# Kernel tuning notes

Measured on AMD Instinct MI355X. Metric: run time of the kernel, lower is better.

The kernel has to match this reference:

```python
import jax, jax.numpy as jnp
import numpy as np

B, N = 4, 20                        # batch, qubits
L = int(np.ceil(np.log2(N)))        # 5 layers, one 4x4 generator each


def setup_inputs():
    key = jax.random.key(0)
    k1, k2, k3, k4 = jax.random.split(key, 4)
    psi_re = jax.random.normal(k1, (B, 2 ** N), dtype=jnp.float32)
    psi_im = jax.random.normal(k2, (B, 2 ** N), dtype=jnp.float32)
    nrm = jnp.sqrt(jnp.sum(psi_re ** 2 + psi_im ** 2, axis=1, keepdims=True))
    psi_re, psi_im = psi_re / nrm, psi_im / nrm   # normalized quantum state
    H_re = jax.random.normal(k3, (L, 4, 4), dtype=jnp.float32)
    H_im = jax.random.normal(k4, (L, 4, 4), dtype=jnp.float32)
    return {"psi_re": psi_re, "psi_im": psi_im, "H_re": H_re, "H_im": H_im}


def _make_unitary(A):
    # torch.matrix_exp(A - A^H): expm of an anti-Hermitian generator via eigh
    G = A - A.conj().T
    w, V = jnp.linalg.eigh(-1j * G)            # G = i * Hermitian
    return (V * jnp.exp(1j * w)) @ V.conj().T  # expm(G), unitary


def _apply_gate(T, U4, axes):
    # contract 4x4 gate (reshaped [2,2,2,2]) onto two qubit axes of tensor T
    T = jnp.tensordot(U4, T, axes=((2, 3), axes))
    return jnp.moveaxis(T, (0, 1), axes)


def _gate_pairs(nq):
    pairs = [(2 * i, 2 * i + 1) for i in range(nq // 2)]
    if nq > 2:
        pairs += [(2 * i + 1, (2 * i + 2) % nq) for i in range(nq // 2)]
    return pairs


def _forward(psi_re, psi_im, H_re, H_im):
    psi = (psi_re + 1j * psi_im).astype(jnp.complex64).reshape((B,) + (2,) * N)
    H = (H_re + 1j * H_im).astype(jnp.complex64)
    state, is_dm, nq = psi, False, N
    for layer in range(L):
        U = _make_unitary(H[layer]).reshape(2, 2, 2, 2)
        Uc = U.conj()
        # _2local_conv: brick pattern of the same 2-qubit gate
        for (a, b) in _gate_pairs(nq):
            state = _apply_gate(state, U, (1 + a, 1 + b))
            if is_dm:  # density matrix: also apply U* on bra axes
                state = _apply_gate(state, Uc, (1 + nq + a, 1 + nq + b))
        # _2local_pool: measuring qubits 0..nq//2-1 with index shifting removes
        # the even-indexed qubits -> partial trace over them
        if nq >= 2:
            traced = [2 * i for i in range(nq // 2)]
            kept = [q for q in range(nq) if q not in traced]
            t, k = len(traced), len(kept)
            if is_dm:
                perm = (0,) + tuple(1 + q for q in kept) + tuple(1 + q for q in traced) \
                     + tuple(1 + nq + q for q in kept) + tuple(1 + nq + q for q in traced)
                r = jnp.transpose(state, perm).reshape(B, 2 ** k, 2 ** t, 2 ** k, 2 ** t)
                state = jnp.einsum('bitjt->bij', r).reshape((B,) + (2,) * k + (2,) * k)
            else:
                perm = (0,) + tuple(1 + q for q in traced) + tuple(1 + q for q in kept)
                p = jnp.transpose(state, perm).reshape(B, 2 ** t, 2 ** k)
                state = jnp.einsum('bti,btj->bij', p, p.conj()).reshape((B,) + (2,) * k + (2,) * k)
                is_dm = True
            nq = k
    # final state.measure(0): reduced 1-qubit density matrix, take P(outcome 0)
    r = state.reshape(B, 2, 2 ** (nq - 1), 2, 2 ** (nq - 1))
    rho0 = jnp.einsum('birjr->bij', r)
    return rho0[:, 0, 0].real


def reference(psi_re, psi_im, H_re, H_im):
    return _forward(psi_re, psi_im, H_re, H_im)
```

## Files before the change

kernel.cpp:

```cpp
#include <hip/hip_runtime.h>
#include <math.h>


typedef float cpx __attribute__((ext_vector_type(2)));

__device__ __forceinline__ cpx mkc(float x, float y) { cpx r; r.x = x; r.y = y; return r; }

__device__ __forceinline__ cpx cmul(cpx a, cpx b) {
  cpx r = a.xx * b;
  return __builtin_elementwise_fma(mkc(-a.y, a.y), b.yx, r);
}
__device__ __forceinline__ cpx cmadd(cpx acc, cpx a, cpx b) {
  acc = __builtin_elementwise_fma(a.xx, b, acc);
  return __builtin_elementwise_fma(mkc(-a.y, a.y), b.yx, acc);
}
__device__ __forceinline__ cpx cmaddc(cpx acc, cpx a, cpx b) {
  acc = __builtin_elementwise_fma(a.xx, mkc(b.x, -b.y), acc);
  return __builtin_elementwise_fma(a.yy, b.yx, acc);
}

__device__ __forceinline__ int pad(int e) { return e + (e >> 4); }
__device__ __forceinline__ int ins(int x, int p) {
  return ((x >> p) << (p + 1)) | (x & ((1 << p) - 1));
}

#define S_STR 36
#define T_STR 1153

__device__ __forceinline__ void gate4(cpx& v0, cpx& v1, cpx& v2, cpx& v3,
                                      const cpx (&U)[16]) {
  cpx n0 = cmul(U[0], v0);  n0 = cmadd(n0, U[1], v1);  n0 = cmadd(n0, U[2], v2);  n0 = cmadd(n0, U[3], v3);
  cpx n1 = cmul(U[4], v0);  n1 = cmadd(n1, U[5], v1);  n1 = cmadd(n1, U[6], v2);  n1 = cmadd(n1, U[7], v3);
  cpx n2 = cmul(U[8], v0);  n2 = cmadd(n2, U[9], v1);  n2 = cmadd(n2, U[10], v2); n2 = cmadd(n2, U[11], v3);
  cpx n3 = cmul(U[12], v0); n3 = cmadd(n3, U[13], v1); n3 = cmadd(n3, U[14], v2); n3 = cmadd(n3, U[15], v3);
  v0 = n0; v1 = n1; v2 = n2; v3 = n3;
}

template <int NG>
__device__ __forceinline__ void gate16n(cpx (&v)[16], const cpx (&U)[16]) {
#pragma unroll
  for (int g = 0; g < 4; g++)
    gate4(v[g * 4 + 0], v[g * 4 + 1], v[g * 4 + 2], v[g * 4 + 3], U);
#pragma unroll
  for (int lo = 0; lo < 4; lo++)
    gate4(v[lo], v[lo + 4], v[lo + 8], v[lo + 12], U);
  if (NG == 3) {
#pragma unroll
    for (int b3 = 0; b3 < 2; b3++)
#pragma unroll
      for (int b0 = 0; b0 < 2; b0++) {
        int j = b3 * 8 + b0;
        gate4(v[j], v[j + 2], v[j + 4], v[j + 6], U);
      }
  }
}

__device__ __forceinline__ void apply_gate_2it(cpx* t, const cpx (&U)[16],
                                               int pa, int pb, int tid) {
  int p0 = pa < pb ? pa : pb;
  int p1 = pa < pb ? pb : pa;
  int m0 = (1 << p0) - 1, m1 = (1 << p1) - 1;
  int ia = 1 << pa, ib = 1 << pb;
#pragma unroll
  for (int g = tid; g < 2048; g += 1024) {
    int idx = ((g & ~m0) << 1) | (g & m0);
    idx = ((idx & ~m1) << 1) | (idx & m1);
    int e0 = pad(idx), e1 = pad(idx | ib), e2 = pad(idx | ia), e3 = pad(idx | ia | ib);
    cpx v0 = t[e0], v1 = t[e1], v2 = t[e2], v3 = t[e3];
    gate4(v0, v1, v2, v3, U);
    t[e0] = v0; t[e1] = v1; t[e2] = v2; t[e3] = v3;
  }
}

__device__ __forceinline__ void phase3_eo(cpx* t, const cpx (&U)[16],
                                          int q0, int q1, int q2,
                                          int o0, int o1, int o2, int tid) {
  int idx = ins(ins(ins(tid, q0), q1), q2);
  cpx v[8];
#pragma unroll
  for (int j = 0; j < 8; j++) {
    int off = ((j & 1) ? o0 : 0) + ((j & 2) ? o1 : 0) + ((j & 4) ? o2 : 0);
    v[j] = t[pad(idx + off)];
  }
  gate4(v[0], v[2], v[4], v[6], U);
  gate4(v[1], v[3], v[5], v[7], U);
  gate4(v[0], v[1], v[2], v[3], U);
  gate4(v[4], v[5], v[6], v[7], U);
#pragma unroll
  for (int j = 0; j < 8; j++) {
    int off = ((j & 1) ? o0 : 0) + ((j & 2) ? o1 : 0) + ((j & 4) ? o2 : 0);
    t[pad(idx + off)] = v[j];
  }
}

template <int NG>
__device__ __forceinline__ void phase4_pool(cpx* w, const cpx (&U)[16],
                                            int a_lo, int a_hi, int c_lo, int c_hi,
                                            int o0, int o1, int o2, int o3, int tid) {
  int uu = tid & 7, ss = (tid >> 3) & 7, t_lo = tid >> 6;
  int u = ins(ins(uu, a_lo), a_hi);
  int s = ins(ins(ss, c_lo), c_hi);
  int base = t_lo * T_STR + s * S_STR + u;
  cpx v[16];
#pragma unroll
  for (int j = 0; j < 16; j++) {
    int off = ((j & 1) ? o0 : 0) + ((j & 2) ? o1 : 0) + ((j & 4) ? o2 : 0) + ((j & 8) ? o3 : 0);
    v[j] = w[base + off];
  }
  gate16n<NG>(v, U);
#pragma unroll
  for (int j = 0; j < 16; j++) {
    int off = ((j & 1) ? o0 : 0) + ((j & 2) ? o1 : 0) + ((j & 4) ? o2 : 0) + ((j & 8) ? o3 : 0);
    w[base + off] = v[j];
  }
}

__device__ __forceinline__ void pool_p3(cpx* w, const cpx (&U)[16], int tid) {
#pragma unroll
  for (int it = 0; it < 2; it++) {
    int h = tid + it * 512;
    int t_lo = h & 7, ss = (h >> 3) & 15, uu = (h >> 7) & 7;
    int base = t_lo * T_STR + (ss << 1) * S_STR + (uu << 2);
    cpx v[8];
    v[0] = w[base];          v[1] = w[base + 1];
    v[4] = w[base + 2];      v[5] = w[base + 3];
    v[2] = w[base + S_STR];      v[3] = w[base + S_STR + 1];
    v[6] = w[base + S_STR + 2];  v[7] = w[base + S_STR + 3];
    gate4(v[0], v[1], v[2], v[3], U);
    gate4(v[4], v[5], v[6], v[7], U);
    gate4(v[0], v[2], v[4], v[6], U);
    gate4(v[1], v[3], v[5], v[7], U);
    w[base] = v[0];          w[base + 1] = v[1];
    w[base + 2] = v[4];      w[base + 3] = v[5];
    w[base + S_STR] = v[2];      w[base + S_STR + 1] = v[3];
    w[base + S_STR + 2] = v[6];  w[base + S_STR + 3] = v[7];
  }
}

__device__ __forceinline__ cpx expm16(const float* __restrict__ Hre,
                                      const float* __restrict__ Him,
                                      int l, int l16) {
  int r = l16 >> 2, c = l16 & 3;
  double tr = (double)Hre[l * 16 + r * 4 + c] - (double)Hre[l * 16 + c * 4 + r];
  double ti = (double)Him[l * 16 + r * 4 + c] + (double)Him[l * 16 + c * 4 + r];
  double a = sqrt(tr * tr + ti * ti);
  a += __shfl_xor(a, 1, 16);
  a += __shfl_xor(a, 2, 16);
  double nrm = fmax(a, __shfl_xor(a, 4, 16));
  nrm = fmax(nrm, __shfl_xor(nrm, 8, 16));
  int s = 0;
  while (nrm > 0.25 && s < 60) { nrm *= 0.5; s++; }
  double sc = ldexp(1.0, -s);
  tr *= sc; ti *= sc;
  double id = (r == c) ? 1.0 : 0.0;
  double er = id, ei = 0.0, pr = id, pi = 0.0;
  for (int k = 1; k <= 16; k++) {
    double qr = 0.0, qi = 0.0;
#pragma unroll
    for (int m = 0; m < 4; m++) {
      double pmr = __shfl(pr, r * 4 + m, 16);
      double pmi = __shfl(pi, r * 4 + m, 16);
      double tmr = __shfl(tr, m * 4 + c, 16);
      double tmi = __shfl(ti, m * 4 + c, 16);
      qr = fma(pmr, tmr, fma(-pmi, tmi, qr));
      qi = fma(pmr, tmi, fma(pmi, tmr, qi));
    }
    double inv = 1.0 / (double)k;
    pr = qr * inv; pi = qi * inv;
    er += pr; ei += pi;
  }
  for (int it = 0; it < s; it++) {
    double qr = 0.0, qi = 0.0;
#pragma unroll
    for (int m = 0; m < 4; m++) {
      double amr = __shfl(er, r * 4 + m, 16);
      double ami = __shfl(ei, r * 4 + m, 16);
      double bmr = __shfl(er, m * 4 + c, 16);
      double bmi = __shfl(ei, m * 4 + c, 16);
      qr = fma(amr, bmr, fma(-ami, bmi, qr));
      qi = fma(amr, bmi, fma(ami, bmr, qi));
    }
    er = qr; ei = qi;
  }
  return mkc((float)er, (float)ei);
}

__global__ __launch_bounds__(128) void compute_U(const float* __restrict__ Hre,
                                                 const float* __restrict__ Him,
                                                 cpx* __restrict__ Umat) {
  int tid = threadIdx.x;
  if (tid < 80) {
    int layer = tid >> 4, l16 = tid & 15;
    Umat[layer * 16 + l16] = expm16(Hre, Him, layer, l16);
  }
}

__global__ __launch_bounds__(1024, 8) void l0_pass1(const float* __restrict__ pre,
                                                    const float* __restrict__ pim,
                                                    const cpx* __restrict__ Umat,
                                                    cpx* __restrict__ state) {
  extern __shared__ cpx tile[];
  int tid = threadIdx.x;
  int bid = blockIdx.x;
  int b = bid >> 7, hi = bid & 127;
  size_t base = ((size_t)b << 20) | ((size_t)hi << 13);
  float4 re[2], im[2];
#pragma unroll
  for (int k = 0; k < 2; k++) {
    int e = (tid + (k << 10)) << 2;
    re[k] = *(const float4*)&pre[base + e];
    im[k] = *(const float4*)&pim[base + e];
  }
#pragma unroll
  for (int k = 0; k < 2; k++) {
    int e = (tid + (k << 10)) << 2;
    int d = pad(e);
    tile[d]     = mkc(re[k].x, im[k].x);
    tile[d + 1] = mkc(re[k].y, im[k].y);
    tile[d + 2] = mkc(re[k].z, im[k].z);
    tile[d + 3] = mkc(re[k].w, im[k].w);
  }
  cpx U[16];
#pragma unroll
  for (int k = 0; k < 16; k++) U[k] = Umat[k];
  __syncthreads();
  apply_gate_2it(tile, U, 1, 0, tid);                 __syncthreads();
  phase3_eo(tile, U, 1, 2, 3, 2, 4, 8, tid);          __syncthreads();
  phase3_eo(tile, U, 3, 4, 5, 8, 16, 32, tid);        __syncthreads();
  phase3_eo(tile, U, 5, 6, 7, 32, 64, 128, tid);      __syncthreads();
  phase3_eo(tile, U, 7, 8, 9, 128, 256, 512, tid);    __syncthreads();
  phase3_eo(tile, U, 9, 10, 11, 512, 1024, 2048, tid);__syncthreads();
  int hifix = ((hi & 1) << 16) | (((hi >> 1) & 1) << 6) | (((hi >> 2) & 1) << 17)
            | (((hi >> 3) & 1) << 5) | (((hi >> 4) & 1) << 18) | (((hi >> 5) & 1) << 7)
            | (((hi >> 6) & 1) << 19);
  size_t dbase = ((size_t)b << 20) | (unsigned)hifix;
  cpx x[8];
#pragma unroll
  for (int k = 0; k < 2; k++) {
    int src = pad((tid + (k << 10)) << 2);
    x[4 * k + 0] = tile[src];     x[4 * k + 1] = tile[src + 1];
    x[4 * k + 2] = tile[src + 2]; x[4 * k + 3] = tile[src + 3];
  }
#pragma unroll
  for (int k = 0; k < 2; k++) {
    int le = tid + (k << 10);
    int d = ((le & 1) << 2) | (((le >> 1) & 1) << 3) | (((le >> 2) & 1) << 8)
          | (((le >> 3) & 1) << 12) | (((le >> 4) & 1) << 10) | (((le >> 5) & 1) << 13)
          | (((le >> 6) & 1) << 9) | (((le >> 7) & 1) << 14) | (((le >> 8) & 1) << 11)
          | (((le >> 9) & 1) << 15) | (((le >> 10) & 1) << 4);
    float4* dst = (float4*)&state[dbase + d];
    dst[0] = make_float4(x[4 * k].x, x[4 * k].y, x[4 * k + 1].x, x[4 * k + 1].y);
    dst[1] = make_float4(x[4 * k + 2].x, x[4 * k + 2].y, x[4 * k + 3].x, x[4 * k + 3].y);
  }
}

__global__ __launch_bounds__(1024, 8) void l0_pass2(const cpx* __restrict__ Umat,
                                                    cpx* __restrict__ state) {
  extern __shared__ cpx tile[];
  int tid = threadIdx.x;
  int bid = blockIdx.x;
  int b = bid >> 7, mid = bid & 127;
  size_t base = ((size_t)b << 20) | ((size_t)mid << 8);
  cpx U[16];
#pragma unroll
  for (int k = 0; k < 16; k++) U[k] = Umat[k];
  {
    float4 v[4];
#pragma unroll
    for (int k = 0; k < 4; k++) {
      int f = tid + (k << 10);
      int run = f >> 7, idx = f & 127;
      v[k] = *(const float4*)&state[base + ((size_t)run << 15) + ((size_t)idx << 1)];
    }
#pragma unroll
    for (int k = 0; k < 4; k++) {
      int f = tid + (k << 10);
      int d = pad((f >> 7) * 256 + (f & 127) * 2);
      tile[d] = mkc(v[k].x, v[k].y);
      tile[d + 1] = mkc(v[k].z, v[k].w);
    }
  }
  __syncthreads();
  phase3_eo(tile, U, 4, 8, 9, 256, 16, 512, tid);     __syncthreads();
  phase3_eo(tile, U, 6, 9, 10, 512, 64, 1024, tid);   __syncthreads();
  phase3_eo(tile, U, 5, 10, 11, 1024, 32, 2048, tid); __syncthreads();
  phase3_eo(tile, U, 7, 11, 12, 2048, 128, 4096, tid);__syncthreads();
  apply_gate_2it(tile, U, 0, 12, tid);                __syncthreads();
  {
    cpx y[8];
#pragma unroll
    for (int k = 0; k < 4; k++) {
      int f = tid + (k << 10);
      int d = pad((f >> 7) * 256 + (f & 127) * 2);
      y[2 * k] = tile[d];
      y[2 * k + 1] = tile[d + 1];
    }
#pragma unroll
    for (int k = 0; k < 4; k++) {
      int f = tid + (k << 10);
      int run = f >> 7, idx = f & 127;
      size_t a = base + ((size_t)run << 15) + ((size_t)idx << 1);
      *(float4*)&state[a] = make_float4(y[2 * k].x, y[2 * k].y, y[2 * k + 1].x, y[2 * k + 1].y);
    }
  }
}

__global__ __launch_bounds__(512, 4) void pool_l1(const cpx* __restrict__ Umat,
                                                  const cpx* __restrict__ state,
                                                  float4* __restrict__ partial) {
  extern __shared__ cpx w[];
  int tid = threadIdx.x;
  int bid = blockIdx.x;
  int b = bid >> 7, thi = bid & 127;
  size_t base = ((size_t)b << 20) | ((size_t)thi << 13);
  cpx U[16];
#pragma unroll
  for (int k = 0; k < 16; k++) U[k] = Umat[16 + k];
  {
    float4 v[8];
#pragma unroll
    for (int k = 0; k < 8; k++) {
      int e = (tid + (k << 9)) << 1;
      v[k] = *(const float4*)&state[base + e];
    }
#pragma unroll
    for (int k = 0; k < 8; k++) {
      int e = (tid + (k << 9)) << 1;
      int u = (((e >> 8) & 1) << 1) | (((e >> 9) & 1) << 2) | (((e >> 4) & 1) << 3) | (((e >> 5) & 1) << 4);
      int s = ((e >> 2) & 1) | (((e >> 10) & 1) << 1) | (((e >> 11) & 1) << 2)
            | (((e >> 6) & 1) << 3) | (((e >> 7) & 1) << 4);
      int t = ((e >> 1) & 1) | (((e >> 3) & 1) << 1) | (((e >> 12) & 1) << 2);
      int c = t * T_STR + s * S_STR + u;
      w[c] = mkc(v[k].x, v[k].y);
      w[c + 1] = mkc(v[k].z, v[k].w);
    }
  }
  __syncthreads();
  phase4_pool<3>(w, U, 3, 4, 3, 4, 8, 8 * S_STR, 16, 16 * S_STR, tid); __syncthreads();
  phase4_pool<3>(w, U, 1, 2, 1, 2, 2, 2 * S_STR, 4, 4 * S_STR, tid);   __syncthreads();
  pool_p3(w, U, tid);                                                  __syncthreads();
  phase4_pool<2>(w, U, 0, 3, 2, 4, 4 * S_STR, 8, 16 * S_STR, 1, tid);  __syncthreads();
  int wv = tid >> 6, lane = tid & 63;
  int u0 = (lane >> 3) << 2, v0 = (lane & 7) << 2;
  cpx acc[4][4];
#pragma unroll
  for (int i = 0; i < 4; i++)
#pragma unroll
    for (int j = 0; j < 4; j++) acc[i][j] = mkc(0.f, 0.f);
  {
    int tb = wv * T_STR;
#pragma unroll 4
    for (int s = 0; s < 32; s++) {
      int row = tb + s * S_STR;
      cpx x[4], y[4];
#pragma unroll
      for (int i = 0; i < 4; i++) { x[i] = w[row + u0 + i]; y[i] = w[row + v0 + i]; }
#pragma unroll
      for (int i = 0; i < 4; i++)
#pragma unroll
        for (int j = 0; j < 4; j++) acc[i][j] = cmaddc(acc[i][j], x[i], y[j]);
    }
  }
  __syncthreads();
#pragma unroll
  for (int i = 0; i < 4; i++)
#pragma unroll
    for (int j = 0; j < 4; j++)
      w[wv * 1024 + (u0 + i) * 32 + (v0 + j)] = acc[i][j];
  __syncthreads();
  {
    cpx s0 = mkc(0.f, 0.f), s1 = mkc(0.f, 0.f);
#pragma unroll
    for (int k = 0; k < 8; k++) {
      s0 += w[k * 1024 + 2 * tid];
      s1 += w[k * 1024 + 2 * tid + 1];
    }
    partial[((size_t)bid << 9) | tid] = make_float4(s0.x, s0.y, s1.x, s1.y);
  }
}

__global__ __launch_bounds__(256) void finish(const cpx* __restrict__ Umat,
                                              const float4* __restrict__ accv,
                                              float* __restrict__ out) {
  __shared__ cpx rho[1024];
  __shared__ cpx r3s[64];
  __shared__ cpx r4s[16];
  int tid = threadIdx.x;
  int b = blockIdx.x;
  float4* rf = (float4*)rho;
  for (int f = tid; f < 512; f += 256) {
    float4 acc = make_float4(0.f, 0.f, 0.f, 0.f);
#pragma unroll 8
    for (int h = 0; h < 128; h++) {
      float4 v = accv[(size_t)(b * 128 + h) * 512 + f];
      acc.x += v.x; acc.y += v.y; acc.z += v.z; acc.w += v.w;
    }
    rf[f] = acc;
  }
  __syncthreads();

  cpx U[16], Uc[16];
#pragma unroll
  for (int k = 0; k < 16; k++) { U[k] = Umat[32 + k]; Uc[k] = mkc(U[k].x, -U[k].y); }
  const int gl2[4][2] = {{4,3},{2,1},{3,2},{1,0}};
#pragma unroll
  for (int gi = 0; gi < 4; gi++) {
    int pa = gl2[gi][0], pb = gl2[gi][1];
    int p0 = pa < pb ? pa : pb, p1 = pa < pb ? pb : pa;
    int m0 = (1 << p0) - 1, m1 = (1 << p1) - 1;
    int ia = 1 << pa, ib = 1 << pb;
    {
      int j = tid >> 3, g = tid & 7;
      int idx = ((g & ~m0) << 1) | (g & m0);
      idx = ((idx & ~m1) << 1) | (idx & m1);
      cpx v0 = rho[idx * 32 + j], v1 = rho[(idx | ib) * 32 + j];
      cpx v2 = rho[(idx | ia) * 32 + j], v3 = rho[(idx | ia | ib) * 32 + j];
      gate4(v0, v1, v2, v3, U);
      rho[idx * 32 + j] = v0; rho[(idx | ib) * 32 + j] = v1;
      rho[(idx | ia) * 32 + j] = v2; rho[(idx | ia | ib) * 32 + j] = v3;
    }
    __syncthreads();
    {
      int i = tid >> 3, g = tid & 7;
      int idx = ((g & ~m0) << 1) | (g & m0);
      idx = ((idx & ~m1) << 1) | (idx & m1);
      cpx v0 = rho[i * 32 + idx], v1 = rho[i * 32 + (idx | ib)];
      cpx v2 = rho[i * 32 + (idx | ia)], v3 = rho[i * 32 + (idx | ia | ib)];
      gate4(v0, v1, v2, v3, Uc);
      rho[i * 32 + idx] = v0; rho[i * 32 + (idx | ib)] = v1;
      rho[i * 32 + (idx | ia)] = v2; rho[i * 32 + (idx | ia | ib)] = v3;
    }
    __syncthreads();
  }
  if (tid < 64) {
    int u = tid >> 3, v = tid & 7;
    cpx acc = mkc(0.f, 0.f);
#pragma unroll
    for (int s = 0; s < 4; s++) {
      int iu = ((s >> 1) << 4) | ((u >> 2) << 3) | ((s & 1) << 2) | (((u >> 1) & 1) << 1) | (u & 1);
      int iv = ((s >> 1) << 4) | ((v >> 2) << 3) | ((s & 1) << 2) | (((v >> 1) & 1) << 1) | (v & 1);
      cpx x = rho[iu * 32 + iv];
      acc.x += x.x; acc.y += x.y;
    }
    r3s[u * 8 + v] = acc;
  }
  __syncthreads();

#pragma unroll
  for (int k = 0; k < 16; k++) { U[k] = Umat[48 + k]; Uc[k] = mkc(U[k].x, -U[k].y); }
  const int gl3[2][2] = {{2,1},{1,0}};
#pragma unroll
  for (int gi = 0; gi < 2; gi++) {
    int pa = gl3[gi][0], pb = gl3[gi][1];
    int p0 = pa < pb ? pa : pb, p1 = pa < pb ? pb : pa;
    int m0 = (1 << p0) - 1, m1 = (1 << p1) - 1;
    int ia = 1 << pa, ib = 1 << pb;
    if (tid < 16) {
      int j = tid >> 1, g = tid & 1;
      int idx = ((g & ~m0) << 1) | (g & m0);
      idx = ((idx & ~m1) << 1) | (idx & m1);
      cpx v0 = r3s[idx * 8 + j], v1 = r3s[(idx | ib) * 8 + j];
      cpx v2 = r3s[(idx | ia) * 8 + j], v3 = r3s[(idx | ia | ib) * 8 + j];
      gate4(v0, v1, v2, v3, U);
      r3s[idx * 8 + j] = v0; r3s[(idx | ib) * 8 + j] = v1;
      r3s[(idx | ia) * 8 + j] = v2; r3s[(idx | ia | ib) * 8 + j] = v3;
    }
    __syncthreads();
    if (tid < 16) {
      int i = tid >> 1, g = tid & 1;
      int idx = ((g & ~m0) << 1) | (g & m0);
      idx = ((idx & ~m1) << 1) | (idx & m1);
      cpx v0 = r3s[i * 8 + idx], v1 = r3s[i * 8 + (idx | ib)];
      cpx v2 = r3s[i * 8 + (idx | ia)], v3 = r3s[i * 8 + (idx | ia | ib)];
      gate4(v0, v1, v2, v3, Uc);
      r3s[i * 8 + idx] = v0; r3s[i * 8 + (idx | ib)] = v1;
      r3s[i * 8 + (idx | ia)] = v2; r3s[i * 8 + (idx | ia | ib)] = v3;
    }
    __syncthreads();
  }
  if (tid < 16) {
    int u = tid >> 2, v = tid & 3;
    cpx acc = mkc(0.f, 0.f);
#pragma unroll
    for (int s = 0; s < 2; s++) {
      cpx x = r3s[((s << 2) | u) * 8 + ((s << 2) | v)];
      acc.x += x.x; acc.y += x.y;
    }
    r4s[u * 4 + v] = acc;
  }
  __syncthreads();

#pragma unroll
  for (int k = 0; k < 16; k++) { U[k] = Umat[64 + k]; Uc[k] = mkc(U[k].x, -U[k].y); }
  if (tid < 4) {
    int j = tid;
    cpx v0 = r4s[0 * 4 + j], v1 = r4s[1 * 4 + j], v2 = r4s[2 * 4 + j], v3 = r4s[3 * 4 + j];
    gate4(v0, v1, v2, v3, U);
    r4s[0 * 4 + j] = v0; r4s[1 * 4 + j] = v1; r4s[2 * 4 + j] = v2; r4s[3 * 4 + j] = v3;
  }
  __syncthreads();
  if (tid < 4) {
    int i = tid;
    cpx v0 = r4s[i * 4 + 0], v1 = r4s[i * 4 + 1], v2 = r4s[i * 4 + 2], v3 = r4s[i * 4 + 3];
    gate4(v0, v1, v2, v3, Uc);
    r4s[i * 4 + 0] = v0; r4s[i * 4 + 1] = v1; r4s[i * 4 + 2] = v2; r4s[i * 4 + 3] = v3;
  }
  __syncthreads();
  if (tid == 0) out[b] = r4s[0].x + r4s[10].x;
}

extern "C" void kernel_launch(void* const* d_in, const int* in_sizes, int n_in,
                              void* d_out, int out_size, void* d_ws, size_t ws_size,
                              hipStream_t stream) {
  const float* psi_re = (const float*)d_in[0];
  const float* psi_im = (const float*)d_in[1];
  const float* H_re = (const float*)d_in[2];
  const float* H_im = (const float*)d_in[3];
  float* out = (float*)d_out;

  char* ws = (char*)d_ws;
  cpx* Umat = (cpx*)ws;
  cpx* state = (cpx*)(ws + 4096);
  float4* partial = (float4*)(ws + 4096 + ((size_t)1 << 25));

  const size_t LDS_L0 = 8704 * sizeof(cpx);
  const size_t LDS_POOL = 8 * T_STR * sizeof(cpx);

  hipLaunchKernelGGL(compute_U, dim3(1), dim3(128), 0, stream, H_re, H_im, Umat);
  hipLaunchKernelGGL(l0_pass1, dim3(512), dim3(1024), LDS_L0, stream,
                     psi_re, psi_im, (const cpx*)Umat, state);
  hipLaunchKernelGGL(l0_pass2, dim3(512), dim3(1024), LDS_L0, stream,
                     (const cpx*)Umat, state);
  hipLaunchKernelGGL(pool_l1, dim3(512), dim3(512), LDS_POOL, stream,
                     (const cpx*)Umat, (const cpx*)state, partial);
  hipLaunchKernelGGL(finish, dim3(4), dim3(256), 0, stream,
                     (const cpx*)Umat, (const float4*)partial, out);
}
```

Measured before the change: 175.9 us.

## Process two tiles per block in layer-0 passes, prefetching the second tile's loads

Both layer-0 kernels now launch 256 blocks, and each block handles two tiles instead of one. The global loads for the second tile are issued into registers before the first tile's gate phases start, so their latency can hide behind LDS compute. This costs extra live registers and lowers the launch-bounds occupancy hint from 8 to 4. With 256 blocks on the device there is also less parallelism to go around.

```diff
diff --git a/kernel.cpp b/kernel.cpp
--- a/kernel.cpp
+++ b/kernel.cpp
@@ -195,41 +195,17 @@
   }
 }
 
-__global__ __launch_bounds__(1024, 8) void l0_pass1(const float* __restrict__ pre,
-                                                    const float* __restrict__ pim,
-                                                    const cpx* __restrict__ Umat,
-                                                    cpx* __restrict__ state) {
-  extern __shared__ cpx tile[];
-  int tid = threadIdx.x;
-  int bid = blockIdx.x;
-  int b = bid >> 7, hi = bid & 127;
-  size_t base = ((size_t)b << 20) | ((size_t)hi << 13);
-  float4 re[2], im[2];
-#pragma unroll
-  for (int k = 0; k < 2; k++) {
-    int e = (tid + (k << 10)) << 2;
-    re[k] = *(const float4*)&pre[base + e];
-    im[k] = *(const float4*)&pim[base + e];
-  }
-#pragma unroll
-  for (int k = 0; k < 2; k++) {
-    int e = (tid + (k << 10)) << 2;
-    int d = pad(e);
-    tile[d]     = mkc(re[k].x, im[k].x);
-    tile[d + 1] = mkc(re[k].y, im[k].y);
-    tile[d + 2] = mkc(re[k].z, im[k].z);
-    tile[d + 3] = mkc(re[k].w, im[k].w);
-  }
-  cpx U[16];
-#pragma unroll
-  for (int k = 0; k < 16; k++) U[k] = Umat[k];
-  __syncthreads();
+__device__ __forceinline__ void p1_phases(cpx* tile, const cpx (&U)[16], int tid) {
   apply_gate_2it(tile, U, 1, 0, tid);                 __syncthreads();
   phase3_eo(tile, U, 1, 2, 3, 2, 4, 8, tid);          __syncthreads();
   phase3_eo(tile, U, 3, 4, 5, 8, 16, 32, tid);        __syncthreads();
   phase3_eo(tile, U, 5, 6, 7, 32, 64, 128, tid);      __syncthreads();
   phase3_eo(tile, U, 7, 8, 9, 128, 256, 512, tid);    __syncthreads();
   phase3_eo(tile, U, 9, 10, 11, 512, 1024, 2048, tid);__syncthreads();
+}
+
+__device__ __forceinline__ void p1_store(cpx* tile, cpx* __restrict__ state,
+                                         int b, int hi, int tid) {
   int hifix = ((hi & 1) << 16) | (((hi >> 1) & 1) << 6) | (((hi >> 2) & 1) << 17)
             | (((hi >> 3) & 1) << 5) | (((hi >> 4) & 1) << 18) | (((hi >> 5) & 1) << 7)
             | (((hi >> 6) & 1) << 19);
@@ -254,38 +230,108 @@
   }
 }
 
-__global__ __launch_bounds__(1024, 8) void l0_pass2(const cpx* __restrict__ Umat,
+__global__ __launch_bounds__(1024, 4) void l0_pass1(const float* __restrict__ pre,
+                                                    const float* __restrict__ pim,
+                                                    const cpx* __restrict__ Umat,
                                                     cpx* __restrict__ state) {
   extern __shared__ cpx tile[];
   int tid = threadIdx.x;
   int bid = blockIdx.x;
-  int b = bid >> 7, mid = bid & 127;
-  size_t base = ((size_t)b << 20) | ((size_t)mid << 8);
+  int t0 = bid, t1 = bid + 256;
+  size_t baseA = ((size_t)(t0 >> 7) << 20) | ((size_t)(t0 & 127) << 13);
+  size_t baseB = ((size_t)(t1 >> 7) << 20) | ((size_t)(t1 & 127) << 13);
   cpx U[16];
 #pragma unroll
   for (int k = 0; k < 16; k++) U[k] = Umat[k];
-  {
-    float4 v[4];
-#pragma unroll
-    for (int k = 0; k < 4; k++) {
-      int f = tid + (k << 10);
-      int run = f >> 7, idx = f & 127;
-      v[k] = *(const float4*)&state[base + ((size_t)run << 15) + ((size_t)idx << 1)];
-    }
-#pragma unroll
-    for (int k = 0; k < 4; k++) {
-      int f = tid + (k << 10);
-      int d = pad((f >> 7) * 256 + (f & 127) * 2);
-      tile[d] = mkc(v[k].x, v[k].y);
-      tile[d + 1] = mkc(v[k].z, v[k].w);
-    }
-  }
-  __syncthreads();
+  float4 reA0, reA1, imA0, imA1;
+  {
+    int e0 = tid << 2, e1 = (tid + 1024) << 2;
+    reA0 = *(const float4*)&pre[baseA + e0];
+    reA1 = *(const float4*)&pre[baseA + e1];
+    imA0 = *(const float4*)&pim[baseA + e0];
+    imA1 = *(const float4*)&pim[baseA + e1];
+  }
+  {
+    int e0 = tid << 2, e1 = (tid + 1024) << 2;
+    int d0 = pad(e0), d1 = pad(e1);
+    tile[d0]     = mkc(reA0.x, imA0.x);
+    tile[d0 + 1] = mkc(reA0.y, imA0.y);
+    tile[d0 + 2] = mkc(reA0.z, imA0.z);
+    tile[d0 + 3] = mkc(reA0.w, imA0.w);
+    tile[d1]     = mkc(reA1.x, imA1.x);
+    tile[d1 + 1] = mkc(reA1.y, imA1.y);
+    tile[d1 + 2] = mkc(reA1.z, imA1.z);
+    tile[d1 + 3] = mkc(reA1.w, imA1.w);
+  }
+  __syncthreads();
+  float4 reB0, reB1, imB0, imB1;
+  {
+    int e0 = tid << 2, e1 = (tid + 1024) << 2;
+    reB0 = *(const float4*)&pre[baseB + e0];
+    reB1 = *(const float4*)&pre[baseB + e1];
+    imB0 = *(const float4*)&pim[baseB + e0];
+    imB1 = *(const float4*)&pim[baseB + e1];
+  }
+  p1_phases(tile, U, tid);
+  p1_store(tile, state, t0 >> 7, t0 & 127, tid);
+  __syncthreads();
+  {
+    int e0 = tid << 2, e1 = (tid + 1024) << 2;
+    int d0 = pad(e0), d1 = pad(e1);
+    tile[d0]     = mkc(reB0.x, imB0.x);
+    tile[d0 + 1] = mkc(reB0.y, imB0.y);
+    tile[d0 + 2] = mkc(reB0.z, imB0.z);
+    tile[d0 + 3] = mkc(reB0.w, imB0.w);
+    tile[d1]     = mkc(reB1.x, imB1.x);
+    tile[d1 + 1] = mkc(reB1.y, imB1.y);
+    tile[d1 + 2] = mkc(reB1.z, imB1.z);
+    tile[d1 + 3] = mkc(reB1.w, imB1.w);
+  }
+  __syncthreads();
+  p1_phases(tile, U, tid);
+  p1_store(tile, state, t1 >> 7, t1 & 127, tid);
+}
+
+__device__ __forceinline__ void p2_phases(cpx* tile, const cpx (&U)[16], int tid) {
   phase3_eo(tile, U, 4, 8, 9, 256, 16, 512, tid);     __syncthreads();
   phase3_eo(tile, U, 6, 9, 10, 512, 64, 1024, tid);   __syncthreads();
   phase3_eo(tile, U, 5, 10, 11, 1024, 32, 2048, tid); __syncthreads();
   phase3_eo(tile, U, 7, 11, 12, 2048, 128, 4096, tid);__syncthreads();
   apply_gate_2it(tile, U, 0, 12, tid);                __syncthreads();
+}
+
+__global__ __launch_bounds__(1024, 4) void l0_pass2(const cpx* __restrict__ Umat,
+                                                    cpx* __restrict__ state) {
+  extern __shared__ cpx tile[];
+  int tid = threadIdx.x;
+  int bid = blockIdx.x;
+  int t0 = bid, t1 = bid + 256;
+  size_t baseA = ((size_t)(t0 >> 7) << 20) | ((size_t)(t0 & 127) << 8);
+  size_t baseB = ((size_t)(t1 >> 7) << 20) | ((size_t)(t1 & 127) << 8);
+  cpx U[16];
+#pragma unroll
+  for (int k = 0; k < 16; k++) U[k] = Umat[k];
+  float4 vA[4];
+#pragma unroll
+  for (int k = 0; k < 4; k++) {
+    int f = tid + (k << 10);
+    vA[k] = *(const float4*)&state[baseA + ((size_t)(f >> 7) << 15) + ((size_t)(f & 127) << 1)];
+  }
+#pragma unroll
+  for (int k = 0; k < 4; k++) {
+    int f = tid + (k << 10);
+    int d = pad((f >> 7) * 256 + (f & 127) * 2);
+    tile[d] = mkc(vA[k].x, vA[k].y);
+    tile[d + 1] = mkc(vA[k].z, vA[k].w);
+  }
+  __syncthreads();
+  float4 vB[4];
+#pragma unroll
+  for (int k = 0; k < 4; k++) {
+    int f = tid + (k << 10);
+    vB[k] = *(const float4*)&state[baseB + ((size_t)(f >> 7) << 15) + ((size_t)(f & 127) << 1)];
+  }
+  p2_phases(tile, U, tid);
   {
     cpx y[8];
 #pragma unroll
@@ -298,8 +344,33 @@
 #pragma unroll
     for (int k = 0; k < 4; k++) {
       int f = tid + (k << 10);
-      int run = f >> 7, idx = f & 127;
-      size_t a = base + ((size_t)run << 15) + ((size_t)idx << 1);
+      size_t a = baseA + ((size_t)(f >> 7) << 15) + ((size_t)(f & 127) << 1);
+      *(float4*)&state[a] = make_float4(y[2 * k].x, y[2 * k].y, y[2 * k + 1].x, y[2 * k + 1].y);
+    }
+  }
+  __syncthreads();
+#pragma unroll
+  for (int k = 0; k < 4; k++) {
+    int f = tid + (k << 10);
+    int d = pad((f >> 7) * 256 + (f & 127) * 2);
+    tile[d] = mkc(vB[k].x, vB[k].y);
+    tile[d + 1] = mkc(vB[k].z, vB[k].w);
+  }
+  __syncthreads();
+  p2_phases(tile, U, tid);
+  {
+    cpx y[8];
+#pragma unroll
+    for (int k = 0; k < 4; k++) {
+      int f = tid + (k << 10);
+      int d = pad((f >> 7) * 256 + (f & 127) * 2);
+      y[2 * k] = tile[d];
+      y[2 * k + 1] = tile[d + 1];
+    }
+#pragma unroll
+    for (int k = 0; k < 4; k++) {
+      int f = tid + (k << 10);
+      size_t a = baseB + ((size_t)(f >> 7) << 15) + ((size_t)(f & 127) << 1);
       *(float4*)&state[a] = make_float4(y[2 * k].x, y[2 * k].y, y[2 * k + 1].x, y[2 * k + 1].y);
     }
   }
@@ -527,9 +598,9 @@
   const size_t LDS_POOL = 8 * T_STR * sizeof(cpx);
 
   hipLaunchKernelGGL(compute_U, dim3(1), dim3(128), 0, stream, H_re, H_im, Umat);
-  hipLaunchKernelGGL(l0_pass1, dim3(512), dim3(1024), LDS_L0, stream,
+  hipLaunchKernelGGL(l0_pass1, dim3(256), dim3(1024), LDS_L0, stream,
                      psi_re, psi_im, (const cpx*)Umat, state);
-  hipLaunchKernelGGL(l0_pass2, dim3(512), dim3(1024), LDS_L0, stream,
+  hipLaunchKernelGGL(l0_pass2, dim3(256), dim3(1024), LDS_L0, stream,
                      (const cpx*)Umat, state);
   hipLaunchKernelGGL(pool_l1, dim3(512), dim3(512), LDS_POOL, stream,
                      (const cpx*)Umat, (const cpx*)state, partial);
```

New measurement: 178.2 us (median of 2 runs). About the same (+1.3%).
